# Performance work log

Measured on AMD Instinct MI355X. Metric: run time of the kernel, lower is better.

## Reference

```python
import jax, jax.numpy as jnp
import numpy as np

K = 1024      # size_codebook
D = 64        # dim_codebook
N = 131072    # number of input vectors
GAMMA = 0.99
ALPHA = 1e-09
BETA = 0.25


def setup_inputs() -> dict:
    key = jax.random.key(0)
    k1, k2, k3 = jax.random.split(key, 3)
    X = jax.random.normal(k1, (N, D), dtype=jnp.float32)
    E = jax.random.normal(k2, (K, D), dtype=jnp.float32)
    cluster_sizes = jnp.zeros((K,), dtype=jnp.float32)
    moving_avg = E  # buffer initialized to a clone of E.weight
    return {"X": X, "E": E, "cluster_sizes": cluster_sizes, "moving_avg": moving_avg}


def reference(X, E, cluster_sizes, moving_avg):
    # squared euclidean distances: [N, K]
    X_sqnorm = jnp.sum(X * X, axis=1, keepdims=True)          # [N, 1]
    E_sqnorm = jnp.sum(E * E, axis=1)[None, :]                # [1, K]
    dist = X_sqnorm + E_sqnorm - 2.0 * (X @ E.T)              # [N, K]
    min_dist = jnp.min(dist, axis=1)                          # [N]
    argmins = jnp.argmin(dist, axis=1)                        # [N]
    Z_embs_raw = E[argmins]                                   # [N, D]

    # commitment loss (codebook is detached in the EMA variant)
    diff = X - jax.lax.stop_gradient(Z_embs_raw)
    loss = BETA * jnp.mean(jnp.sum(diff * diff, axis=1))

    # EMA codebook update (training mode, no-grad in torch)
    counts = jax.ops.segment_sum(jnp.ones((N,), dtype=X.dtype), argmins, num_segments=K)
    cs = GAMMA * cluster_sizes + (1.0 - GAMMA) * counts
    cs = (cs + ALPHA) / (1.0 + ALPHA * K / jnp.sum(cs))
    sums = jax.ops.segment_sum(X, argmins, num_segments=K)    # one_hot.T @ X, [K, D]
    ma = GAMMA * moving_avg + (1.0 - GAMMA) * sums
    E_new = ma / cs[:, None]

    # straight-through estimator
    Z_embs = X + jax.lax.stop_gradient(Z_embs_raw - X)
    return (Z_embs, loss, argmins, min_dist, E_new, cs, ma)
```

## Files before the change

### kernel.cpp

```cpp
#include <hip/hip_runtime.h>
#include <math.h>

#define NN 131072
#define KK 1024
#define DD 64
#define GAMMA 0.99f
#define ALPHA 1e-9f
#define BETA 0.25f

typedef float f32x4 __attribute__((ext_vector_type(4)));
typedef short bf16x8 __attribute__((ext_vector_type(8)));

typedef const __attribute__((address_space(1))) void gv_t;
typedef __attribute__((address_space(3))) void lv_t;

__device__ __constant__ float OMG = (float)(1.0 - 0.99);

__device__ __forceinline__ void split_bf16(float v, unsigned short& h, unsigned short& l) {
    unsigned int b = __float_as_uint(v);
    unsigned int hb = b & 0xFFFF0000u;
    h = (unsigned short)(hb >> 16);
    float r = v - __uint_as_float(hb);
    unsigned int lb = __float_as_uint(r);
    lb += 0x7FFFu + ((lb >> 16) & 1u);
    l = (unsigned short)(lb >> 16);
}

__global__ __launch_bounds__(64)
void vq_prep(const float* __restrict__ E, float4* __restrict__ Efrag,
             float* __restrict__ esqh) {
    int nt = blockIdx.x;
    int l = threadIdx.x;
    int n = nt * 16 + (l & 15);
    int kb = (l >> 4) * 8;
    float ss = 0.f;
    #pragma unroll
    for (int ks = 0; ks < 2; ++ks) {
        const float4* xp = (const float4*)(E + (size_t)n * DD + ks * 32 + kb);
        float4 a = xp[0], b = xp[1];
        float v[8] = {a.x, a.y, a.z, a.w, b.x, b.y, b.z, b.w};
        union { float4 f; unsigned short u[8]; } H, L;
        #pragma unroll
        for (int j = 0; j < 8; ++j) {
            unsigned short hh, ll;
            split_bf16(v[j], hh, ll);
            H.u[j] = hh; L.u[j] = ll;
            ss = fmaf(v[j], v[j], ss);
        }
        int fid = nt * 4 + ks * 2;
        Efrag[(size_t)(fid + 0) * 64 + l] = H.f;
        Efrag[(size_t)(fid + 1) * 64 + l] = L.f;
    }
    ss += __shfl_xor(ss, 16, 64);
    ss += __shfl_xor(ss, 32, 64);
    if (l < 16) esqh[nt * 16 + l] = -0.5f * ss;
}

#define BM 64

__global__ __launch_bounds__(256, 4)
void vq_main(const float* __restrict__ X, const float* __restrict__ E,
             const float4* __restrict__ Efrag, const float* __restrict__ esqh,
             float* __restrict__ argf, float* __restrict__ mind,
             float* __restrict__ Z, int* __restrict__ cursor,
             int* __restrict__ rowlist, float* __restrict__ sumsFB,
             float* __restrict__ loss_part, int cap) {
    __shared__ float4 stg[2][8][64];
    __shared__ float redv[128];
    __shared__ int redi[128];
    __shared__ int bidx[64];
    __shared__ float bsc[64];
    __shared__ float xsqs[64];
    __shared__ int fbflag[64];

    int tid = threadIdx.x;
    int lane = tid & 63, w = tid >> 6;
    int rg = w & 1, cg = w >> 1;
    int lc = lane & 15, lq = lane >> 4;

    size_t bb = (size_t)blockIdx.x * BM;
    size_t R0 = bb + rg * 32;

    int st = (blockIdx.x >> 3) & 31;

    auto stage_tile = [&](float4 (*sb)[64], int nt) {
        int cgs = w >> 1, fp = (w & 1) * 2;
        const float4* gp = Efrag + ((size_t)(cgs * 32 + nt)) * 256 + fp * 64 + lane;
        __builtin_amdgcn_global_load_lds((gv_t*)gp,
                                         (lv_t*)&sb[cgs * 4 + fp][0], 16, 0, 0);
        __builtin_amdgcn_global_load_lds((gv_t*)(gp + 64),
                                         (lv_t*)&sb[cgs * 4 + fp + 1][0], 16, 0, 0);
    };

    stage_tile(stg[0], st);

    bf16x8 ah[2][2], al[2][2];
    #pragma unroll
    for (int mt = 0; mt < 2; ++mt) {
        float xq = 0.f;
        #pragma unroll
        for (int ks = 0; ks < 2; ++ks) {
            const float4* xp =
                (const float4*)(X + (R0 + mt * 16 + lc) * DD + ks * 32 + lq * 8);
            float4 x0 = xp[0], x1 = xp[1];
            float v[8] = {x0.x, x0.y, x0.z, x0.w, x1.x, x1.y, x1.z, x1.w};
            union { bf16x8 s; unsigned short u[8]; } H, L;
            #pragma unroll
            for (int j = 0; j < 8; ++j) {
                unsigned short hh, ll;
                split_bf16(v[j], hh, ll);
                H.u[j] = hh; L.u[j] = ll;
                xq = fmaf(v[j], v[j], xq);
            }
            ah[mt][ks] = H.s;
            al[mt][ks] = L.s;
        }
        xq += __shfl_xor(xq, 16, 64);
        xq += __shfl_xor(xq, 32, 64);
        if (lane < 16) xsqs[rg * 32 + mt * 16 + lane] = xq;
    }

    float bestv[2][4];
    int besti[2][4];
    #pragma unroll
    for (int mt = 0; mt < 2; ++mt)
        #pragma unroll
        for (int r = 0; r < 4; ++r) { bestv[mt][r] = -3.402823466e38f; besti[mt][r] = 0; }

    const float* ep = esqh + cg * 512 + lc;

    auto consume = [&](float4 (*sb)[64], int ntp) {
        float ec = ep[ntp * 16];
        union { float4 f; bf16x8 s; } u0, u1, u2, u3;
        u0.f = sb[cg * 4 + 0][lane];
        u1.f = sb[cg * 4 + 1][lane];
        u2.f = sb[cg * 4 + 2][lane];
        u3.f = sb[cg * 4 + 3][lane];
        f32x4 acc[2];
        #pragma unroll
        for (int mt = 0; mt < 2; ++mt) acc[mt] = (f32x4){ec, ec, ec, ec};
        #pragma unroll
        for (int mt = 0; mt < 2; ++mt)
            acc[mt] = __builtin_amdgcn_mfma_f32_16x16x32_bf16(ah[mt][0], u0.s, acc[mt], 0, 0, 0);
        #pragma unroll
        for (int mt = 0; mt < 2; ++mt)
            acc[mt] = __builtin_amdgcn_mfma_f32_16x16x32_bf16(ah[mt][1], u2.s, acc[mt], 0, 0, 0);
        #pragma unroll
        for (int mt = 0; mt < 2; ++mt)
            acc[mt] = __builtin_amdgcn_mfma_f32_16x16x32_bf16(ah[mt][0], u1.s, acc[mt], 0, 0, 0);
        #pragma unroll
        for (int mt = 0; mt < 2; ++mt)
            acc[mt] = __builtin_amdgcn_mfma_f32_16x16x32_bf16(ah[mt][1], u3.s, acc[mt], 0, 0, 0);
        #pragma unroll
        for (int mt = 0; mt < 2; ++mt)
            acc[mt] = __builtin_amdgcn_mfma_f32_16x16x32_bf16(al[mt][0], u0.s, acc[mt], 0, 0, 0);
        #pragma unroll
        for (int mt = 0; mt < 2; ++mt)
            acc[mt] = __builtin_amdgcn_mfma_f32_16x16x32_bf16(al[mt][1], u2.s, acc[mt], 0, 0, 0);
        int n = cg * 512 + ntp * 16 + lc;
        #pragma unroll
        for (int mt = 0; mt < 2; ++mt)
            #pragma unroll
            for (int r = 0; r < 4; ++r) {
                float sc = acc[mt][r];
                if (sc > bestv[mt][r]) { bestv[mt][r] = sc; besti[mt][r] = n; }
            }
    };

    for (int i = 0; i < 32; i += 2) {
        __syncthreads();
        stage_tile(stg[1], (i + 1 + st) & 31);
        consume(stg[0], (i + st) & 31);
        __syncthreads();
        if (i + 2 < 32) stage_tile(stg[0], (i + 2 + st) & 31);
        consume(stg[1], (i + 1 + st) & 31);
    }

    #pragma unroll
    for (int off = 1; off <= 8; off <<= 1) {
        #pragma unroll
        for (int mt = 0; mt < 2; ++mt) {
            #pragma unroll
            for (int r = 0; r < 4; ++r) {
                float ov = __shfl_xor(bestv[mt][r], off, 64);
                int oi = __shfl_xor(besti[mt][r], off, 64);
                if (ov > bestv[mt][r] || (ov == bestv[mt][r] && oi < besti[mt][r])) {
                    bestv[mt][r] = ov; besti[mt][r] = oi;
                }
            }
        }
    }
    if (lc == 0) {
        #pragma unroll
        for (int mt = 0; mt < 2; ++mt)
            #pragma unroll
            for (int r = 0; r < 4; ++r) {
                int row = rg * 32 + mt * 16 + lq * 4 + r;
                redv[row * 2 + cg] = bestv[mt][r];
                redi[row * 2 + cg] = besti[mt][r];
            }
    }
    __syncthreads();
    if (tid < 64) {
        float v0 = redv[tid * 2], v1 = redv[tid * 2 + 1];
        int i0 = redi[tid * 2], i1 = redi[tid * 2 + 1];
        int pick = (v1 > v0 || (v1 == v0 && i1 < i0));
        bidx[tid] = pick ? i1 : i0;
        bsc[tid] = pick ? v1 : v0;
    }
    __syncthreads();

    if (tid < 64) {
        int row = tid;
        int bi = bidx[row];
        size_t grow = bb + row;
        float md = fmaf(-2.f, bsc[row], xsqs[row]);
        mind[grow] = md;
        argf[grow] = (float)bi;
        int pos = atomicAdd(&cursor[bi], 1);
        if (pos < cap) {
            rowlist[(size_t)bi * cap + pos] = (int)grow;
            fbflag[row] = 0;
        } else {
            fbflag[row] = 1;
        }
        #pragma unroll
        for (int m = 32; m; m >>= 1) md += __shfl_xor(md, m, 64);
        if (tid == 0) atomicAdd(&loss_part[blockIdx.x & 1023], md);
    }
    __syncthreads();

    #pragma unroll 4
    for (int it = 0; it < 16; ++it) {
        int row = w * 16 + it;
        int bi = bidx[row];
        size_t grow = bb + row;
        float e = E[(size_t)bi * DD + lane];
        Z[grow * DD + lane] = e;
        if (fbflag[row]) {
            float x = X[grow * DD + lane];
            atomicAdd(&sumsFB[(size_t)bi * DD + lane], x);
        }
    }
}

__global__ __launch_bounds__(1024)
void vq_sum_ema(const float* __restrict__ X, const int* __restrict__ rowlist,
                const int* __restrict__ cursor, const float* __restrict__ sumsFB,
                const float* __restrict__ cluster_sizes,
                const float* __restrict__ loss_part, const float* __restrict__ mavg,
                float* __restrict__ o_ma, float* __restrict__ o_enew,
                float* __restrict__ o_cs, float* __restrict__ o_loss, int cap) {
    __shared__ float part[16][64];
    __shared__ float redt[16];
    int k = blockIdx.x;
    int lane = threadIdx.x & 63, w = threadIdx.x >> 6;

    float t = GAMMA * cluster_sizes[threadIdx.x] + OMG * (float)cursor[threadIdx.x];
    #pragma unroll
    for (int m = 32; m; m >>= 1) t += __shfl_xor(t, m, 64);
    if (lane == 0) redt[w] = t;
    __syncthreads();
    float total = 0.f;
    #pragma unroll
    for (int j = 0; j < 16; ++j) total += redt[j];

    float csr = GAMMA * cluster_sizes[k] + OMG * (float)cursor[k];
    float cs = (csr + ALPHA) / (1.0f + (ALPHA * (float)KK) / total);
    if (threadIdx.x == 0) o_cs[k] = cs;

    if (k == 0) {
        __syncthreads();
        float t2 = loss_part[threadIdx.x];
        #pragma unroll
        for (int m = 32; m; m >>= 1) t2 += __shfl_xor(t2, m, 64);
        if (lane == 0) redt[w] = t2;
        __syncthreads();
        if (threadIdx.x == 0) {
            float l = 0.f;
            #pragma unroll
            for (int j = 0; j < 16; ++j) l += redt[j];
            o_loss[0] = BETA * (l / (float)NN);
        }
    }

    int cnt = cursor[k];
    int nr = cnt < cap ? cnt : cap;
    const int* rl = rowlist + (size_t)k * cap;
    float acc = 0.f;
    #pragma unroll 4
    for (int i = w; i < nr; i += 16) {
        int r = rl[i];
        acc += X[(size_t)r * DD + lane];
    }
    part[w][lane] = acc;
    __syncthreads();
    if (w == 0) {
        float s = sumsFB[(size_t)k * DD + lane];
        #pragma unroll
        for (int j = 0; j < 16; ++j) s += part[j][lane];
        float ma = GAMMA * mavg[(size_t)k * DD + lane] + OMG * s;
        o_ma[(size_t)k * DD + lane] = ma;
        o_enew[(size_t)k * DD + lane] = ma / cs;
    }
}

extern "C" void kernel_launch(void* const* d_in, const int* in_sizes, int n_in,
                              void* d_out, int out_size, void* d_ws, size_t ws_size,
                              hipStream_t stream) {
    const float* X = (const float*)d_in[0];
    const float* E = (const float*)d_in[1];
    const float* cluster_sizes = (const float*)d_in[2];
    const float* moving_avg = (const float*)d_in[3];

    float* out = (float*)d_out;
    float* o_Z = out;
    float* o_loss = o_Z + (size_t)NN * DD;
    float* o_arg = o_loss + 1;
    float* o_mind = o_arg + NN;
    float* o_enew = o_mind + NN;
    float* o_cs = o_enew + (size_t)KK * DD;
    float* o_ma = o_cs + KK;

    int* cursor = (int*)d_ws;
    float* loss_part = (float*)d_ws + 1024;
    float* sumsFB = loss_part + 1024;
    float* esqh = sumsFB + (size_t)KK * DD;
    float4* Efrag = (float4*)(esqh + KK);
    int* rowlist = (int*)(esqh + KK + (size_t)KK * DD);

    size_t base_bytes = (size_t)(1024 + 1024 + KK * DD + KK + KK * DD) * 4;
    long cap_l = ((long)ws_size - (long)base_bytes) / (long)(KK * sizeof(int));
    int cap = cap_l < 0 ? 0 : (cap_l > 1024 ? 1024 : (int)cap_l);

    hipMemsetAsync(d_ws, 0, (size_t)(1024 + 1024 + KK * DD) * 4, stream);

    vq_prep<<<KK / 16, 64, 0, stream>>>(E, Efrag, esqh);
    vq_main<<<NN / BM, 256, 0, stream>>>(X, E, Efrag, esqh, o_arg, o_mind, o_Z,
                                         cursor, rowlist, sumsFB, loss_part, cap);
    vq_sum_ema<<<KK, 1024, 0, stream>>>(X, rowlist, cursor, sumsFB, cluster_sizes,
                                        loss_part, moving_avg, o_ma, o_enew,
                                        o_cs, o_loss, cap);
}
```

Measured before the change: 202.8 us.

## Replace row-list gather with direct atomic accumulation of cluster sums

The per-cluster row lists and the follow-up gather kernel are removed. The main kernel now atomically adds every input row into a global sums buffer, and a small EMA kernel finishes the update with one wave per cluster. This drops the second pass over X and the scattered row-index reads, at the cost of N*D float atomics in the main kernel. Those atomics may contend on popular clusters, and the summation order becomes nondeterministic.

```diff
diff --git a/kernel.cpp b/kernel.cpp
--- a/kernel.cpp
+++ b/kernel.cpp
@@ -63,15 +63,13 @@
              const float4* __restrict__ Efrag, const float* __restrict__ esqh,
              float* __restrict__ argf, float* __restrict__ mind,
              float* __restrict__ Z, int* __restrict__ cursor,
-             int* __restrict__ rowlist, float* __restrict__ sumsFB,
-             float* __restrict__ loss_part, int cap) {
+             float* __restrict__ sums, float* __restrict__ loss_part) {
     __shared__ float4 stg[2][8][64];
     __shared__ float redv[128];
     __shared__ int redi[128];
     __shared__ int bidx[64];
     __shared__ float bsc[64];
     __shared__ float xsqs[64];
-    __shared__ int fbflag[64];
 
     int tid = threadIdx.x;
     int lane = tid & 63, w = tid >> 6;
@@ -217,13 +215,7 @@
         float md = fmaf(-2.f, bsc[row], xsqs[row]);
         mind[grow] = md;
         argf[grow] = (float)bi;
-        int pos = atomicAdd(&cursor[bi], 1);
-        if (pos < cap) {
-            rowlist[(size_t)bi * cap + pos] = (int)grow;
-            fbflag[row] = 0;
-        } else {
-            fbflag[row] = 1;
-        }
+        atomicAdd(&cursor[bi], 1);
         #pragma unroll
         for (int m = 32; m; m >>= 1) md += __shfl_xor(md, m, 64);
         if (tid == 0) atomicAdd(&loss_part[blockIdx.x & 1023], md);
@@ -236,72 +228,54 @@
         int bi = bidx[row];
         size_t grow = bb + row;
         float e = E[(size_t)bi * DD + lane];
+        float x = X[grow * DD + lane];
         Z[grow * DD + lane] = e;
-        if (fbflag[row]) {
-            float x = X[grow * DD + lane];
-            atomicAdd(&sumsFB[(size_t)bi * DD + lane], x);
-        }
-    }
-}
-
-__global__ __launch_bounds__(1024)
-void vq_sum_ema(const float* __restrict__ X, const int* __restrict__ rowlist,
-                const int* __restrict__ cursor, const float* __restrict__ sumsFB,
-                const float* __restrict__ cluster_sizes,
-                const float* __restrict__ loss_part, const float* __restrict__ mavg,
-                float* __restrict__ o_ma, float* __restrict__ o_enew,
-                float* __restrict__ o_cs, float* __restrict__ o_loss, int cap) {
-    __shared__ float part[16][64];
-    __shared__ float redt[16];
-    int k = blockIdx.x;
-    int lane = threadIdx.x & 63, w = threadIdx.x >> 6;
-
-    float t = GAMMA * cluster_sizes[threadIdx.x] + OMG * (float)cursor[threadIdx.x];
+        atomicAdd(&sums[(size_t)bi * DD + lane], x);
+    }
+}
+
+__global__ __launch_bounds__(256)
+void vq_ema(const int* __restrict__ cursor, const float* __restrict__ sums,
+            const float* __restrict__ cluster_sizes,
+            const float* __restrict__ loss_part, const float* __restrict__ mavg,
+            float* __restrict__ o_ma, float* __restrict__ o_enew,
+            float* __restrict__ o_cs, float* __restrict__ o_loss) {
+    __shared__ float redt[4];
+    int tid = threadIdx.x, lane = tid & 63, w = tid >> 6;
+    int k = blockIdx.x * 4 + w;
+
+    float t = 0.f;
+    #pragma unroll
+    for (int j = 0; j < 4; ++j) {
+        int c = tid + j * 256;
+        t += GAMMA * cluster_sizes[c] + OMG * (float)cursor[c];
+    }
     #pragma unroll
     for (int m = 32; m; m >>= 1) t += __shfl_xor(t, m, 64);
     if (lane == 0) redt[w] = t;
     __syncthreads();
-    float total = 0.f;
-    #pragma unroll
-    for (int j = 0; j < 16; ++j) total += redt[j];
+    float total = redt[0] + redt[1] + redt[2] + redt[3];
 
     float csr = GAMMA * cluster_sizes[k] + OMG * (float)cursor[k];
     float cs = (csr + ALPHA) / (1.0f + (ALPHA * (float)KK) / total);
-    if (threadIdx.x == 0) o_cs[k] = cs;
-
-    if (k == 0) {
+    if (lane == 0) o_cs[k] = cs;
+
+    float s = sums[(size_t)k * DD + lane];
+    float ma = GAMMA * mavg[(size_t)k * DD + lane] + OMG * s;
+    o_ma[(size_t)k * DD + lane] = ma;
+    o_enew[(size_t)k * DD + lane] = ma / cs;
+
+    if (blockIdx.x == 0) {
+        float l = 0.f;
+        #pragma unroll
+        for (int j = 0; j < 4; ++j) l += loss_part[tid + j * 256];
+        #pragma unroll
+        for (int m = 32; m; m >>= 1) l += __shfl_xor(l, m, 64);
         __syncthreads();
-        float t2 = loss_part[threadIdx.x];
-        #pragma unroll
-        for (int m = 32; m; m >>= 1) t2 += __shfl_xor(t2, m, 64);
-        if (lane == 0) redt[w] = t2;
+        if (lane == 0) redt[w] = l;
         __syncthreads();
-        if (threadIdx.x == 0) {
-            float l = 0.f;
-            #pragma unroll
-            for (int j = 0; j < 16; ++j) l += redt[j];
-            o_loss[0] = BETA * (l / (float)NN);
-        }
-    }
-
-    int cnt = cursor[k];
-    int nr = cnt < cap ? cnt : cap;
-    const int* rl = rowlist + (size_t)k * cap;
-    float acc = 0.f;
-    #pragma unroll 4
-    for (int i = w; i < nr; i += 16) {
-        int r = rl[i];
-        acc += X[(size_t)r * DD + lane];
-    }
-    part[w][lane] = acc;
-    __syncthreads();
-    if (w == 0) {
-        float s = sumsFB[(size_t)k * DD + lane];
-        #pragma unroll
-        for (int j = 0; j < 16; ++j) s += part[j][lane];
-        float ma = GAMMA * mavg[(size_t)k * DD + lane] + OMG * s;
-        o_ma[(size_t)k * DD + lane] = ma;
-        o_enew[(size_t)k * DD + lane] = ma / cs;
+        if (tid == 0)
+            o_loss[0] = BETA * ((redt[0] + redt[1] + redt[2] + redt[3]) / (float)NN);
     }
 }
 
@@ -324,21 +298,15 @@
 
     int* cursor = (int*)d_ws;
     float* loss_part = (float*)d_ws + 1024;
-    float* sumsFB = loss_part + 1024;
-    float* esqh = sumsFB + (size_t)KK * DD;
+    float* sums = loss_part + 1024;
+    float* esqh = sums + (size_t)KK * DD;
     float4* Efrag = (float4*)(esqh + KK);
-    int* rowlist = (int*)(esqh + KK + (size_t)KK * DD);
-
-    size_t base_bytes = (size_t)(1024 + 1024 + KK * DD + KK + KK * DD) * 4;
-    long cap_l = ((long)ws_size - (long)base_bytes) / (long)(KK * sizeof(int));
-    int cap = cap_l < 0 ? 0 : (cap_l > 1024 ? 1024 : (int)cap_l);
 
     hipMemsetAsync(d_ws, 0, (size_t)(1024 + 1024 + KK * DD) * 4, stream);
 
     vq_prep<<<KK / 16, 64, 0, stream>>>(E, Efrag, esqh);
     vq_main<<<NN / BM, 256, 0, stream>>>(X, E, Efrag, esqh, o_arg, o_mind, o_Z,
-                                         cursor, rowlist, sumsFB, loss_part, cap);
-    vq_sum_ema<<<KK, 1024, 0, stream>>>(X, rowlist, cursor, sumsFB, cluster_sizes,
-                                        loss_part, moving_avg, o_ma, o_enew,
-                                        o_cs, o_loss, cap);
-}
+                                         cursor, sums, loss_part);
+    vq_ema<<<KK / 4, 256, 0, stream>>>(cursor, sums, cluster_sizes, loss_part,
+                                       moving_avg, o_ma, o_enew, o_cs, o_loss);
+}
```

New measurement: 227.7 us. 1.12x slower.

## Process codebook tile pairs per barrier and fold workspace zeroing into prep

Applied to the files above, without the earlier changes.

The main distance loop now stages and consumes two 16-code tiles per iteration, which halves the number of block barriers and interleaves two independent MFMA accumulator chains. This doubles the LDS staging buffer and lowers the occupancy hint from 4 to 3 blocks per CU. The separate hipMemsetAsync of the workspace is removed, and the prep kernel now zeroes it, saving one launch/memset. The risks are higher register and LDS pressure and fewer resident waves.

```diff
diff --git a/kernel.cpp b/kernel.cpp
--- a/kernel.cpp
+++ b/kernel.cpp
@@ -26,9 +26,14 @@
     l = (unsigned short)(lb >> 16);
 }
 
+#define WSZERO (1024 + 1024 + KK * DD)
+
 __global__ __launch_bounds__(64)
 void vq_prep(const float* __restrict__ E, float4* __restrict__ Efrag,
-             float* __restrict__ esqh) {
+             float* __restrict__ esqh, int* __restrict__ wsz) {
+    int gtid = blockIdx.x * 64 + threadIdx.x;
+    for (int i = gtid; i < WSZERO; i += 64 * (KK / 16)) wsz[i] = 0;
+
     int nt = blockIdx.x;
     int l = threadIdx.x;
     int n = nt * 16 + (l & 15);
@@ -58,14 +63,14 @@
 
 #define BM 64
 
-__global__ __launch_bounds__(256, 4)
+__global__ __launch_bounds__(256, 3)
 void vq_main(const float* __restrict__ X, const float* __restrict__ E,
              const float4* __restrict__ Efrag, const float* __restrict__ esqh,
              float* __restrict__ argf, float* __restrict__ mind,
              float* __restrict__ Z, int* __restrict__ cursor,
              int* __restrict__ rowlist, float* __restrict__ sumsFB,
              float* __restrict__ loss_part, int cap) {
-    __shared__ float4 stg[2][8][64];
+    __shared__ float4 stg[2][2][8][64];
     __shared__ float redv[128];
     __shared__ int redi[128];
     __shared__ int bidx[64];
@@ -83,16 +88,17 @@
 
     int st = (blockIdx.x >> 3) & 31;
 
-    auto stage_tile = [&](float4 (*sb)[64], int nt) {
-        int cgs = w >> 1, fp = (w & 1) * 2;
-        const float4* gp = Efrag + ((size_t)(cgs * 32 + nt)) * 256 + fp * 64 + lane;
-        __builtin_amdgcn_global_load_lds((gv_t*)gp,
-                                         (lv_t*)&sb[cgs * 4 + fp][0], 16, 0, 0);
-        __builtin_amdgcn_global_load_lds((gv_t*)(gp + 64),
-                                         (lv_t*)&sb[cgs * 4 + fp + 1][0], 16, 0, 0);
+    auto stage_pair = [&](float4 (*sb)[8][64], int t0, int t1) {
+        int ti = w >> 1, cgs = w & 1;
+        int nt = (ti ? t1 : t0) & 31;
+        const float4* gp = Efrag + ((size_t)(cgs * 32 + nt)) * 256 + lane;
+        #pragma unroll
+        for (int j = 0; j < 4; ++j)
+            __builtin_amdgcn_global_load_lds((gv_t*)(gp + j * 64),
+                                             (lv_t*)&sb[ti][cgs * 4 + j][0], 16, 0, 0);
     };
 
-    stage_tile(stg[0], st);
+    stage_pair(stg[0], st, st + 1);
 
     bf16x8 ah[2][2], al[2][2];
     #pragma unroll
@@ -129,51 +135,69 @@
 
     const float* ep = esqh + cg * 512 + lc;
 
-    auto consume = [&](float4 (*sb)[64], int ntp) {
-        float ec = ep[ntp * 16];
-        union { float4 f; bf16x8 s; } u0, u1, u2, u3;
-        u0.f = sb[cg * 4 + 0][lane];
-        u1.f = sb[cg * 4 + 1][lane];
-        u2.f = sb[cg * 4 + 2][lane];
-        u3.f = sb[cg * 4 + 3][lane];
-        f32x4 acc[2];
-        #pragma unroll
-        for (int mt = 0; mt < 2; ++mt) acc[mt] = (f32x4){ec, ec, ec, ec};
+    auto consume_pair = [&](float4 (*sb)[8][64], int ntp0, int ntp1) {
+        float ec0 = ep[ntp0 * 16], ec1 = ep[ntp1 * 16];
+        union { float4 f; bf16x8 s; } u[4], v[4];
+        #pragma unroll
+        for (int j = 0; j < 4; ++j) {
+            u[j].f = sb[0][cg * 4 + j][lane];
+            v[j].f = sb[1][cg * 4 + j][lane];
+        }
+        f32x4 acc[2][2];
+        #pragma unroll
+        for (int mt = 0; mt < 2; ++mt) {
+            acc[0][mt] = (f32x4){ec0, ec0, ec0, ec0};
+            acc[1][mt] = (f32x4){ec1, ec1, ec1, ec1};
+        }
+        #pragma unroll
+        for (int mt = 0; mt < 2; ++mt) {
+            acc[0][mt] = __builtin_amdgcn_mfma_f32_16x16x32_bf16(ah[mt][0], u[0].s, acc[0][mt], 0, 0, 0);
+            acc[1][mt] = __builtin_amdgcn_mfma_f32_16x16x32_bf16(ah[mt][0], v[0].s, acc[1][mt], 0, 0, 0);
+        }
+        #pragma unroll
+        for (int mt = 0; mt < 2; ++mt) {
+            acc[0][mt] = __builtin_amdgcn_mfma_f32_16x16x32_bf16(ah[mt][1], u[2].s, acc[0][mt], 0, 0, 0);
+            acc[1][mt] = __builtin_amdgcn_mfma_f32_16x16x32_bf16(ah[mt][1], v[2].s, acc[1][mt], 0, 0, 0);
+        }
+        #pragma unroll
+        for (int mt = 0; mt < 2; ++mt) {
+            acc[0][mt] = __builtin_amdgcn_mfma_f32_16x16x32_bf16(ah[mt][0], u[1].s, acc[0][mt], 0, 0, 0);
+            acc[1][mt] = __builtin_amdgcn_mfma_f32_16x16x32_bf16(ah[mt][0], v[1].s, acc[1][mt], 0, 0, 0);
+        }
+        #pragma unroll
+        for (int mt = 0; mt < 2; ++mt) {
+            acc[0][mt] = __builtin_amdgcn_mfma_f32_16x16x32_bf16(ah[mt][1], u[3].s, acc[0][mt], 0, 0, 0);
+            acc[1][mt] = __builtin_amdgcn_mfma_f32_16x16x32_bf16(ah[mt][1], v[3].s, acc[1][mt], 0, 0, 0);
+        }
+        #pragma unroll
+        for (int mt = 0; mt < 2; ++mt) {
+            acc[0][mt] = __builtin_amdgcn_mfma_f32_16x16x32_bf16(al[mt][0], u[0].s, acc[0][mt], 0, 0, 0);
+            acc[1][mt] = __builtin_amdgcn_mfma_f32_16x16x32_bf16(al[mt][0], v[0].s, acc[1][mt], 0, 0, 0);
+        }
+        #pragma unroll
+        for (int mt = 0; mt < 2; ++mt) {
+            acc[0][mt] = __builtin_amdgcn_mfma_f32_16x16x32_bf16(al[mt][1], u[2].s, acc[0][mt], 0, 0, 0);
+            acc[1][mt] = __builtin_amdgcn_mfma_f32_16x16x32_bf16(al[mt][1], v[2].s, acc[1][mt], 0, 0, 0);
+        }
+        int n0 = cg * 512 + ntp0 * 16 + lc;
+        int n1 = cg * 512 + ntp1 * 16 + lc;
         #pragma unroll
         for (int mt = 0; mt < 2; ++mt)
-            acc[mt] = __builtin_amdgcn_mfma_f32_16x16x32_bf16(ah[mt][0], u0.s, acc[mt], 0, 0, 0);
-        #pragma unroll
-        for (int mt = 0; mt < 2; ++mt)
-            acc[mt] = __builtin_amdgcn_mfma_f32_16x16x32_bf16(ah[mt][1], u2.s, acc[mt], 0, 0, 0);
-        #pragma unroll
-        for (int mt = 0; mt < 2; ++mt)
-            acc[mt] = __builtin_amdgcn_mfma_f32_16x16x32_bf16(ah[mt][0], u1.s, acc[mt], 0, 0, 0);
-        #pragma unroll
-        for (int mt = 0; mt < 2; ++mt)
-            acc[mt] = __builtin_amdgcn_mfma_f32_16x16x32_bf16(ah[mt][1], u3.s, acc[mt], 0, 0, 0);
-        #pragma unroll
-        for (int mt = 0; mt < 2; ++mt)
-            acc[mt] = __builtin_amdgcn_mfma_f32_16x16x32_bf16(al[mt][0], u0.s, acc[mt], 0, 0, 0);
-        #pragma unroll
-        for (int mt = 0; mt < 2; ++mt)
-            acc[mt] = __builtin_amdgcn_mfma_f32_16x16x32_bf16(al[mt][1], u2.s, acc[mt], 0, 0, 0);
-        int n = cg * 512 + ntp * 16 + lc;
-        #pragma unroll
-        for (int mt = 0; mt < 2; ++mt)
             #pragma unroll
             for (int r = 0; r < 4; ++r) {
-                float sc = acc[mt][r];
-                if (sc > bestv[mt][r]) { bestv[mt][r] = sc; besti[mt][r] = n; }
+                float s0 = acc[0][mt][r];
+                if (s0 > bestv[mt][r]) { bestv[mt][r] = s0; besti[mt][r] = n0; }
+                float s1 = acc[1][mt][r];
+                if (s1 > bestv[mt][r]) { bestv[mt][r] = s1; besti[mt][r] = n1; }
             }
     };
 
-    for (int i = 0; i < 32; i += 2) {
+    #pragma unroll 2
+    for (int p = 0; p < 16; ++p) {
+        int cur = p & 1;
         __syncthreads();
-        stage_tile(stg[1], (i + 1 + st) & 31);
-        consume(stg[0], (i + st) & 31);
-        __syncthreads();
-        if (i + 2 < 32) stage_tile(stg[0], (i + 2 + st) & 31);
-        consume(stg[1], (i + 1 + st) & 31);
+        if (p < 15) stage_pair(stg[cur ^ 1], st + 2 * p + 2, st + 2 * p + 3);
+        consume_pair(stg[cur], (st + 2 * p) & 31, (st + 2 * p + 1) & 31);
     }
 
     #pragma unroll
@@ -333,9 +357,7 @@
     long cap_l = ((long)ws_size - (long)base_bytes) / (long)(KK * sizeof(int));
     int cap = cap_l < 0 ? 0 : (cap_l > 1024 ? 1024 : (int)cap_l);
 
-    hipMemsetAsync(d_ws, 0, (size_t)(1024 + 1024 + KK * DD) * 4, stream);
-
-    vq_prep<<<KK / 16, 64, 0, stream>>>(E, Efrag, esqh);
+    vq_prep<<<KK / 16, 64, 0, stream>>>(E, Efrag, esqh, cursor);
     vq_main<<<NN / BM, 256, 0, stream>>>(X, E, Efrag, esqh, o_arg, o_mind, o_Z,
                                          cursor, rowlist, sumsFB, loss_part, cap);
     vq_sum_ema<<<KK, 1024, 0, stream>>>(X, rowlist, cursor, sumsFB, cluster_sizes,
```

Result: no change. 199.9 us (-1.4%).

## Deepen codebook staging to 4-stage ring, cache esq in LDS, fold memset into prep

Applied to the files above, without the earlier changes.

The main kernel's double-buffered LDS staging of codebook fragments becomes a 4-deep ring with three tiles in flight. Explicit vmcnt waits and one barrier per tile replace the two full syncthreads per pair. The half squared norms are loaded once into LDS instead of read from global on every tile. The workspace memset is folded into the prep kernel to save a launch. The extra LDS (about 36KB per block) may reduce occupancy below the 4 blocks requested by launch bounds.

```diff
diff --git a/kernel.cpp b/kernel.cpp
--- a/kernel.cpp
+++ b/kernel.cpp
@@ -26,9 +26,14 @@
     l = (unsigned short)(lb >> 16);
 }
 
+#define WSZERO (1024 + 1024 + KK * DD)
+
 __global__ __launch_bounds__(64)
 void vq_prep(const float* __restrict__ E, float4* __restrict__ Efrag,
-             float* __restrict__ esqh) {
+             float* __restrict__ esqh, int* __restrict__ wsz) {
+    int gtid = blockIdx.x * 64 + threadIdx.x;
+    for (int i = gtid; i < WSZERO; i += 64 * (KK / 16)) wsz[i] = 0;
+
     int nt = blockIdx.x;
     int l = threadIdx.x;
     int n = nt * 16 + (l & 15);
@@ -65,7 +70,8 @@
              float* __restrict__ Z, int* __restrict__ cursor,
              int* __restrict__ rowlist, float* __restrict__ sumsFB,
              float* __restrict__ loss_part, int cap) {
-    __shared__ float4 stg[2][8][64];
+    __shared__ float4 stg[4][8][64];
+    __shared__ float eld[1024];
     __shared__ float redv[128];
     __shared__ int redi[128];
     __shared__ int bidx[64];
@@ -93,6 +99,10 @@
     };
 
     stage_tile(stg[0], st);
+    stage_tile(stg[1], (st + 1) & 31);
+    stage_tile(stg[2], (st + 2) & 31);
+
+    for (int i = tid; i < 1024; i += 256) eld[i] = esqh[i];
 
     bf16x8 ah[2][2], al[2][2];
     #pragma unroll
@@ -127,10 +137,8 @@
         #pragma unroll
         for (int r = 0; r < 4; ++r) { bestv[mt][r] = -3.402823466e38f; besti[mt][r] = 0; }
 
-    const float* ep = esqh + cg * 512 + lc;
-
     auto consume = [&](float4 (*sb)[64], int ntp) {
-        float ec = ep[ntp * 16];
+        float ec = eld[cg * 512 + ntp * 16 + lc];
         union { float4 f; bf16x8 s; } u0, u1, u2, u3;
         u0.f = sb[cg * 4 + 0][lane];
         u1.f = sb[cg * 4 + 1][lane];
@@ -167,14 +175,25 @@
             }
     };
 
-    for (int i = 0; i < 32; i += 2) {
-        __syncthreads();
-        stage_tile(stg[1], (i + 1 + st) & 31);
-        consume(stg[0], (i + st) & 31);
-        __syncthreads();
-        if (i + 2 < 32) stage_tile(stg[0], (i + 2 + st) & 31);
-        consume(stg[1], (i + 1 + st) & 31);
-    }
+    for (int t = 0; t < 29; ++t) {
+        asm volatile("s_waitcnt vmcnt(4)" ::: "memory");
+        __builtin_amdgcn_s_barrier();
+        __builtin_amdgcn_sched_barrier(0);
+        stage_tile(stg[(t + 3) & 3], (st + t + 3) & 31);
+        consume(stg[t & 3], (st + t) & 31);
+    }
+    asm volatile("s_waitcnt vmcnt(4)" ::: "memory");
+    __builtin_amdgcn_s_barrier();
+    __builtin_amdgcn_sched_barrier(0);
+    consume(stg[29 & 3], (st + 29) & 31);
+    asm volatile("s_waitcnt vmcnt(2)" ::: "memory");
+    __builtin_amdgcn_s_barrier();
+    __builtin_amdgcn_sched_barrier(0);
+    consume(stg[30 & 3], (st + 30) & 31);
+    asm volatile("s_waitcnt vmcnt(0)" ::: "memory");
+    __builtin_amdgcn_s_barrier();
+    __builtin_amdgcn_sched_barrier(0);
+    consume(stg[31 & 3], (st + 31) & 31);
 
     #pragma unroll
     for (int off = 1; off <= 8; off <<= 1) {
@@ -333,9 +352,7 @@
     long cap_l = ((long)ws_size - (long)base_bytes) / (long)(KK * sizeof(int));
     int cap = cap_l < 0 ? 0 : (cap_l > 1024 ? 1024 : (int)cap_l);
 
-    hipMemsetAsync(d_ws, 0, (size_t)(1024 + 1024 + KK * DD) * 4, stream);
-
-    vq_prep<<<KK / 16, 64, 0, stream>>>(E, Efrag, esqh);
+    vq_prep<<<KK / 16, 64, 0, stream>>>(E, Efrag, esqh, cursor);
     vq_main<<<NN / BM, 256, 0, stream>>>(X, E, Efrag, esqh, o_arg, o_mind, o_Z,
                                          cursor, rowlist, sumsFB, loss_part, cap);
     vq_sum_ema<<<KK, 1024, 0, stream>>>(X, rowlist, cursor, sumsFB, cluster_sizes,
```

After: 207.4 us. +2.2%, slower.
